# Performance work log

Hardware: AMD Instinct MI355X
Metric: run time of the kernel (lower is better)

## Reference

```python
import jax, jax.numpy as jnp
import numpy as np
from jax.scipy.special import gammaln

WARMUP = 365
KERNEL = 15
PRECISION = 1e-5

# [lo, hi] per parameter, order: BETA FC K0 K1 K2 LP PERC UZL TT CFMAX CFR CWH A THETA
PARAM_RANGES = np.array([
    [1.0, 6.0], [50.0, 1000.0], [0.05, 0.9], [0.01, 0.5], [0.001, 0.2],
    [0.2, 1.0], [0.0, 10.0], [0.0, 100.0], [-2.5, 2.5], [0.5, 10.0],
    [0.0, 0.1], [0.0, 0.2], [0.0, 2.9], [0.0, 6.5],
], dtype=np.float32)


def scale_params(parameters):
    lo = jnp.asarray(PARAM_RANGES[:, 0])
    hi = jnp.asarray(PARAM_RANGES[:, 1])
    return lo + parameters * (hi - lo)  # [n_grid, 14]


def run_hbv(p_all, pet_all, t_all, phys, init_state):
    beta, fc, k0, k1, k2 = phys[:, 0], phys[:, 1], phys[:, 2], phys[:, 3], phys[:, 4]
    lp, pperc, uzl, tt = phys[:, 5], phys[:, 6], phys[:, 7], phys[:, 8]
    cfmax, cfr, cwh = phys[:, 9], phys[:, 10], phys[:, 11]

    def step(state, inp):
        snowpack, meltwater, sm, suz, slz = state
        precip, potent, tempre = inp
        is_rain = (tempre >= tt).astype(jnp.float32)
        rain = precip * is_rain
        snow = precip * (1.0 - is_rain)
        snowpack = snowpack + snow
        melt = jnp.minimum(jnp.maximum(cfmax * (tempre - tt), 0.0), snowpack)
        meltwater = meltwater + melt
        snowpack = snowpack - melt
        refreezing = jnp.minimum(jnp.maximum(cfr * cfmax * (tt - tempre), 0.0), meltwater)
        snowpack = snowpack + refreezing
        meltwater = meltwater - refreezing
        to_soil = jnp.maximum(meltwater - cwh * snowpack, 0.0)
        meltwater = meltwater - to_soil
        soil_wetness = jnp.clip((sm / fc) ** beta, 0.0, 1.0)
        recharge = (rain + to_soil) * soil_wetness
        sm = sm + rain + to_soil - recharge
        excess = jnp.maximum(sm - fc, 0.0)
        sm = sm - excess
        evap_factor = jnp.clip(sm / (lp * fc), 0.0, 1.0)
        et_act = jnp.minimum(sm, potent * evap_factor)
        sm = jnp.maximum(sm - et_act, PRECISION)
        suz = suz + recharge + excess
        perc = jnp.minimum(suz, pperc)
        suz = suz - perc
        q0 = k0 * jnp.maximum(suz - uzl, 0.0)
        suz = suz - q0
        q1 = k1 * suz
        suz = suz - q1
        slz = slz + perc
        q2 = k2 * slz
        slz = slz - q2
        return (snowpack, meltwater, sm, suz, slz), q0 + q1 + q2

    final_state, q_sim = jax.lax.scan(step, init_state, (p_all, pet_all, t_all))
    return q_sim, final_state


def uh_gamma(a, b, len_uh):
    # a, b: [n_grid]; returns normalized gamma-pdf unit hydrograph [len_uh, n_grid]
    aa = jax.nn.relu(a) + 0.1
    theta = jax.nn.relu(b) + 0.5
    t = jnp.arange(0.5, len_uh, dtype=jnp.float32)[:, None]  # [K, 1]
    log_w = (aa - 1.0) * jnp.log(t) - t / theta - gammaln(aa) - aa * jnp.log(theta)
    w = jnp.exp(log_w)
    return w / w.sum(axis=0, keepdims=True)


def hbv_forward(x, parameters):
    n_grid = x.shape[1]
    phys = scale_params(parameters)
    init = tuple(jnp.full((n_grid,), 0.001, dtype=jnp.float32) for _ in range(5))
    # warmup under no_grad -> stop_gradient on resulting states
    xw = x[:WARMUP]
    _, warm_state = run_hbv(xw[..., 0], xw[..., 1], xw[..., 2], phys, init)
    warm_state = jax.lax.stop_gradient(warm_state)
    xm = x[WARMUP:]
    q_sim, _ = run_hbv(xm[..., 0], xm[..., 1], xm[..., 2], phys, warm_state)  # [n_step, n_grid]
    # gamma unit-hydrograph routing (causal conv over time, per grid cell)
    uh = uh_gamma(phys[:, 12], phys[:, 13], KERNEL)  # [K, n_grid]
    n_step = q_sim.shape[0]
    qp = jnp.pad(q_sim, ((KERNEL - 1, 0), (0, 0)))
    qs = jnp.zeros_like(q_sim)
    for k in range(KERNEL):
        qs = qs + uh[k] * jax.lax.dynamic_slice_in_dim(qp, KERNEL - 1 - k, n_step, 0)
    return qs[..., None]  # [n_step, n_grid, 1]


def setup_inputs() -> dict:
    key = jax.random.key(0)
    k1, k2, k3, k4 = jax.random.split(key, 4)
    T, G = 2190, 10000  # 365 warmup + 1825 simulated days, 10k basins
    precip = jax.random.uniform(k1, (T, G), dtype=jnp.float32) * 10.0  # mm/day
    pet = jax.random.uniform(k2, (T, G), dtype=jnp.float32) * 5.0      # mm/day
    temp = jax.random.normal(k3, (T, G), dtype=jnp.float32) * 10.0     # deg C
    x = jnp.stack([precip, pet, temp], axis=-1)
    parameters = jax.random.uniform(k4, (G, 14), dtype=jnp.float32)
    return {"x": x, "parameters": parameters}


def reference(x, parameters):
    return hbv_forward(x, parameters)
```

## Files before the change

### kernel.cpp

```cpp
#include <hip/hip_runtime.h>

#define WARMUP  365
#define NSTEP   1825
#define TTOT    2190
#define KERNEL_ 15
#define CH      5

__global__ __launch_bounds__(64) void hbv_fused_kernel(
    const float* __restrict__ x,
    const float* __restrict__ params,
    float* __restrict__ out,
    int G)
{
    const int g = blockIdx.x * 64 + threadIdx.x;
    if (g >= G) return;

    const float* pr = params + (size_t)g * 14;
    const float beta  = 1.0f   + pr[0]  * 5.0f;
    const float fc    = 50.0f  + pr[1]  * 950.0f;
    const float k0    = 0.05f  + pr[2]  * 0.85f;
    const float k1    = 0.01f  + pr[3]  * 0.49f;
    const float k2    = 0.001f + pr[4]  * 0.199f;
    const float lp    = 0.2f   + pr[5]  * 0.8f;
    const float pperc =          pr[6]  * 10.0f;
    const float uzl   =          pr[7]  * 100.0f;
    const float tt    = -2.5f  + pr[8]  * 5.0f;
    const float cfmax = 0.5f   + pr[9]  * 9.5f;
    const float cfr   =          pr[10] * 0.1f;
    const float cwh   =          pr[11] * 0.2f;
    const float ra    =          pr[12] * 2.9f;
    const float rb    =          pr[13] * 6.5f;

    const float aa = fmaxf(ra, 0.0f) + 0.1f;
    const float th = fmaxf(rb, 0.0f) + 0.5f;
    const float inv_th = 1.0f / th;
    float w[KERNEL_];
    float ws = 0.0f;
    #pragma unroll
    for (int k = 0; k < KERNEL_; k++) {
        const float tk = 0.5f + (float)k;
        const float lw = (aa - 1.0f) * __logf(tk) - tk * inv_th;
        w[k] = __expf(lw);
        ws += w[k];
    }
    const float inv_ws = 1.0f / ws;
    #pragma unroll
    for (int k = 0; k < KERNEL_; k++) w[k] *= inv_ws;

    const float inv_fc   = 1.0f / fc;
    const float inv_lpfc = 1.0f / (lp * fc);
    const float cfrx     = cfr * cfmax;

    float sp  = 0.001f;
    float mw  = 0.001f;
    float sm  = 0.001f;
    float suz = 0.001f;
    float slz = 0.001f;

    auto step = [&](float precip, float pet, float temp) -> float {
        const float rain = (temp >= tt) ? precip : 0.0f;
        const float snow = precip - rain;
        sp += snow;
        const float melt = fminf(fmaxf(cfmax * (temp - tt), 0.0f), sp);
        mw += melt;
        sp -= melt;
        const float refr = fminf(fmaxf(cfrx * (tt - temp), 0.0f), mw);
        sp += refr;
        mw -= refr;
        const float tosoil = fmaxf(mw - cwh * sp, 0.0f);
        mw -= tosoil;
        const float r   = sm * inv_fc;
        float wet = __expf(beta * __logf(r));
        wet = fminf(wet, 1.0f);
        const float inflow = rain + tosoil;
        const float rech   = inflow * wet;
        sm += inflow - rech;
        const float exc = fmaxf(sm - fc, 0.0f);
        sm -= exc;
        const float ef = fminf(sm * inv_lpfc, 1.0f);
        const float et = fminf(sm, pet * ef);
        sm = fmaxf(sm - et, 1e-5f);
        suz += rech + exc;
        const float perc = fminf(suz, pperc);
        suz -= perc;
        const float q0 = k0 * fmaxf(suz - uzl, 0.0f);
        suz -= q0;
        const float q1 = k1 * suz;
        suz -= q1;
        slz += perc;
        const float q2 = k2 * slz;
        slz -= q2;
        return q0 + q1 + q2;
    };

    float cur[CH][3];
    #pragma unroll
    for (int i = 0; i < CH; i++) {
        const float* p = x + ((size_t)i * G + g) * 3;
        cur[i][0] = p[0]; cur[i][1] = p[1]; cur[i][2] = p[2];
    }

    for (int tc = 0; tc < WARMUP; tc += CH) {
        float nxt[CH][3];
        #pragma unroll
        for (int i = 0; i < CH; i++) {
            const float* p = x + ((size_t)(tc + CH + i) * G + g) * 3;
            nxt[i][0] = p[0]; nxt[i][1] = p[1]; nxt[i][2] = p[2];
        }
        #pragma unroll
        for (int i = 0; i < CH; i++)
            (void)step(cur[i][0], cur[i][1], cur[i][2]);
        #pragma unroll
        for (int i = 0; i < CH; i++) {
            cur[i][0] = nxt[i][0]; cur[i][1] = nxt[i][1]; cur[i][2] = nxt[i][2];
        }
    }

    float buf[KERNEL_];
    #pragma unroll
    for (int k = 0; k < KERNEL_; k++) buf[k] = 0.0f;

    for (int tc = WARMUP; tc < TTOT; tc += CH) {
        float nxt[CH][3];
        #pragma unroll
        for (int i = 0; i < CH; i++) {
            int tn = tc + CH + i;
            if (tn > TTOT - 1) tn = TTOT - 1;
            const float* p = x + ((size_t)tn * G + g) * 3;
            nxt[i][0] = p[0]; nxt[i][1] = p[1]; nxt[i][2] = p[2];
        }
        #pragma unroll
        for (int i = 0; i < CH; i++) {
            const float q = step(cur[i][0], cur[i][1], cur[i][2]);
            #pragma unroll
            for (int k = KERNEL_ - 1; k > 0; k--) buf[k] = buf[k - 1];
            buf[0] = q;
            float acc = 0.0f;
            #pragma unroll
            for (int k = 0; k < KERNEL_; k++) acc = fmaf(w[k], buf[k], acc);
            out[(size_t)(tc - WARMUP + i) * G + g] = acc;
        }
        #pragma unroll
        for (int i = 0; i < CH; i++) {
            cur[i][0] = nxt[i][0]; cur[i][1] = nxt[i][1]; cur[i][2] = nxt[i][2];
        }
    }
}

extern "C" void kernel_launch(void* const* d_in, const int* in_sizes, int n_in,
                              void* d_out, int out_size, void* d_ws, size_t ws_size,
                              hipStream_t stream) {
    const float* x      = (const float*)d_in[0];
    const float* params = (const float*)d_in[1];
    float* out = (float*)d_out;
    const int G = in_sizes[1] / 14;
    const int blocks = (G + 63) / 64;
    hbv_fused_kernel<<<blocks, 64, 0, stream>>>(x, params, out, G);
}
```

Measured before the change: 661.9 us.

## Double-buffer 15-step input blocks and use scatter-accumulate routing ring

Replaces the 5-step prefetch with a 15-step double-buffered load scheme (A/B register blocks of 45 floats), unifying warmup and simulation into one loop of 30-step chunks. The routing convolution becomes a rotating accumulator ring updated by scattering w[k]*q forward, with constant indices under full unroll instead of a shift register and dot product. It also uses exp2/log2 builtins, folds the evapotranspiration clamp algebraically, and sets launch_bounds(64,1). The larger register footprint may cut occupancy, and the big unroll raises code size.

```diff
diff --git a/kernel.cpp b/kernel.cpp
--- a/kernel.cpp
+++ b/kernel.cpp
@@ -1,12 +1,85 @@
 #include <hip/hip_runtime.h>
 
-#define WARMUP  365
-#define NSTEP   1825
-#define TTOT    2190
-#define KERNEL_ 15
-#define CH      5
+#define WARMUP 365
+#define NSTEP  1825
+#define TTOT   2190
+#define KER    15
 
-__global__ __launch_bounds__(64) void hbv_fused_kernel(
+#define EXP2F(v) __builtin_exp2f(v)
+#define LOG2F(v) __builtin_log2f(v)
+
+#define LOADBLK(BUF, T0)                                                    \
+    do {                                                                    \
+        _Pragma("unroll")                                                   \
+        for (int j_ = 0; j_ < 15; j_++) {                                   \
+            const float* p_ = x + ((size_t)((T0) + j_) * G + g) * 3;        \
+            BUF[3 * j_ + 0] = p_[0];                                        \
+            BUF[3 * j_ + 1] = p_[1];                                        \
+            BUF[3 * j_ + 2] = p_[2];                                        \
+        }                                                                   \
+    } while (0)
+
+#define RUNBLK(BUF, TB)                                                     \
+    do {                                                                    \
+        _Pragma("unroll")                                                   \
+        for (int j = 0; j < 15; j++) {                                      \
+            const float pcp = BUF[3 * j + 0];                               \
+            const float pet = BUF[3 * j + 1];                               \
+            const float tmp = BUF[3 * j + 2];                               \
+                      \
+            const float dtemp   = tmp - tt;                                 \
+            const float rain    = (tmp >= tt) ? pcp : 0.0f;                 \
+            const float snow    = pcp - rain;                               \
+            const float meltcap = fmaxf(cfmax * dtemp, 0.0f);               \
+            const float refrcap = fmaxf(-cfrx * dtemp, 0.0f);               \
+            const float pl      = pet * inv_lpfc;                           \
+                                                       \
+            sp += snow;                                                     \
+            const float melt = fminf(meltcap, sp);                          \
+            mw += melt;                                                     \
+            sp -= melt;                                                     \
+            const float refr = fminf(refrcap, mw);                          \
+            sp += refr;                                                     \
+            mw -= refr;                                                     \
+            const float tosoil = fmaxf(mw - cwh * sp, 0.0f);                \
+            mw -= tosoil;                                                   \
+                                                         \
+            const float wet =                                               \
+                fminf(EXP2F(beta * LOG2F(sm * inv_fc)), 1.0f);              \
+            const float inflow = rain + tosoil;                             \
+            const float rech   = inflow * wet;                              \
+            const float smx    = sm + inflow;                               \
+            sm = smx - rech;                                                \
+            const float exc = fmaxf(sm - fc, 0.0f);                         \
+            sm = fminf(sm, fc);                                             \
+            const float et = fminf(sm, fminf(pl * sm, pet));                \
+            sm = fmaxf(sm - et, 1e-5f);                                     \
+                                                   \
+            suz += rech + exc;                                              \
+            const float perc = fminf(suz, pperc);                           \
+            suz -= perc;                                                    \
+            const float q0 = k0 * fmaxf(suz - uzl, 0.0f);                   \
+            suz -= q0;                                                      \
+            const float q1 = k1 * suz;                                      \
+            suz -= q1;                                                      \
+            slz += perc;                                                    \
+            const float q2 = k2 * slz;                                      \
+            slz -= q2;                                                      \
+            const float q = q0 + q1 + q2;                                   \
+                    \
+            if ((TB) + j >= WARMUP) {                                       \
+                const int s_ = (j + 10) % 15;                               \
+                out[(size_t)((TB) + j - WARMUP) * G + g] =                  \
+                    acc[s_] + w[0] * q;                                     \
+                acc[s_] = 0.0f;                                             \
+                _Pragma("unroll")                                           \
+                for (int k = 1; k < 15; k++)                                \
+                    acc[(s_ + k) % 15] += w[k] * q;                         \
+            }                                                               \
+        }                                                                   \
+    } while (0)
+
+__global__ __launch_bounds__(64, 1) void hbv_fused_kernel(
     const float* __restrict__ x,
     const float* __restrict__ params,
     float* __restrict__ out,
@@ -33,19 +106,19 @@
 
     const float aa = fmaxf(ra, 0.0f) + 0.1f;
     const float th = fmaxf(rb, 0.0f) + 0.5f;
-    const float inv_th = 1.0f / th;
-    float w[KERNEL_];
+    const float c1 = aa - 1.0f;
+    const float c2 = 1.4426950408889634f / th;
+    float w[KER];
     float ws = 0.0f;
     #pragma unroll
-    for (int k = 0; k < KERNEL_; k++) {
+    for (int k = 0; k < KER; k++) {
         const float tk = 0.5f + (float)k;
-        const float lw = (aa - 1.0f) * __logf(tk) - tk * inv_th;
-        w[k] = __expf(lw);
+        w[k] = EXP2F(c1 * LOG2F(tk) - tk * c2);
         ws += w[k];
     }
     const float inv_ws = 1.0f / ws;
     #pragma unroll
-    for (int k = 0; k < KERNEL_; k++) w[k] *= inv_ws;
+    for (int k = 0; k < KER; k++) w[k] *= inv_ws;
 
     const float inv_fc   = 1.0f / fc;
     const float inv_lpfc = 1.0f / (lp * fc);
@@ -57,93 +130,19 @@
     float suz = 0.001f;
     float slz = 0.001f;
 
-    auto step = [&](float precip, float pet, float temp) -> float {
-        const float rain = (temp >= tt) ? precip : 0.0f;
-        const float snow = precip - rain;
-        sp += snow;
-        const float melt = fminf(fmaxf(cfmax * (temp - tt), 0.0f), sp);
-        mw += melt;
-        sp -= melt;
-        const float refr = fminf(fmaxf(cfrx * (tt - temp), 0.0f), mw);
-        sp += refr;
-        mw -= refr;
-        const float tosoil = fmaxf(mw - cwh * sp, 0.0f);
-        mw -= tosoil;
-        const float r   = sm * inv_fc;
-        float wet = __expf(beta * __logf(r));
-        wet = fminf(wet, 1.0f);
-        const float inflow = rain + tosoil;
-        const float rech   = inflow * wet;
-        sm += inflow - rech;
-        const float exc = fmaxf(sm - fc, 0.0f);
-        sm -= exc;
-        const float ef = fminf(sm * inv_lpfc, 1.0f);
-        const float et = fminf(sm, pet * ef);
-        sm = fmaxf(sm - et, 1e-5f);
-        suz += rech + exc;
-        const float perc = fminf(suz, pperc);
-        suz -= perc;
-        const float q0 = k0 * fmaxf(suz - uzl, 0.0f);
-        suz -= q0;
-        const float q1 = k1 * suz;
-        suz -= q1;
-        slz += perc;
-        const float q2 = k2 * slz;
-        slz -= q2;
-        return q0 + q1 + q2;
-    };
+    float acc[KER];
+    #pragma unroll
+    for (int k = 0; k < KER; k++) acc[k] = 0.0f;
 
-    float cur[CH][3];
-    #pragma unroll
-    for (int i = 0; i < CH; i++) {
-        const float* p = x + ((size_t)i * G + g) * 3;
-        cur[i][0] = p[0]; cur[i][1] = p[1]; cur[i][2] = p[2];
-    }
-
-    for (int tc = 0; tc < WARMUP; tc += CH) {
-        float nxt[CH][3];
-        #pragma unroll
-        for (int i = 0; i < CH; i++) {
-            const float* p = x + ((size_t)(tc + CH + i) * G + g) * 3;
-            nxt[i][0] = p[0]; nxt[i][1] = p[1]; nxt[i][2] = p[2];
-        }
-        #pragma unroll
-        for (int i = 0; i < CH; i++)
-            (void)step(cur[i][0], cur[i][1], cur[i][2]);
-        #pragma unroll
-        for (int i = 0; i < CH; i++) {
-            cur[i][0] = nxt[i][0]; cur[i][1] = nxt[i][1]; cur[i][2] = nxt[i][2];
-        }
-    }
-
-    float buf[KERNEL_];
-    #pragma unroll
-    for (int k = 0; k < KERNEL_; k++) buf[k] = 0.0f;
-
-    for (int tc = WARMUP; tc < TTOT; tc += CH) {
-        float nxt[CH][3];
-        #pragma unroll
-        for (int i = 0; i < CH; i++) {
-            int tn = tc + CH + i;
-            if (tn > TTOT - 1) tn = TTOT - 1;
-            const float* p = x + ((size_t)tn * G + g) * 3;
-            nxt[i][0] = p[0]; nxt[i][1] = p[1]; nxt[i][2] = p[2];
-        }
-        #pragma unroll
-        for (int i = 0; i < CH; i++) {
-            const float q = step(cur[i][0], cur[i][1], cur[i][2]);
-            #pragma unroll
-            for (int k = KERNEL_ - 1; k > 0; k--) buf[k] = buf[k - 1];
-            buf[0] = q;
-            float acc = 0.0f;
-            #pragma unroll
-            for (int k = 0; k < KERNEL_; k++) acc = fmaf(w[k], buf[k], acc);
-            out[(size_t)(tc - WARMUP + i) * G + g] = acc;
-        }
-        #pragma unroll
-        for (int i = 0; i < CH; i++) {
-            cur[i][0] = nxt[i][0]; cur[i][1] = nxt[i][1]; cur[i][2] = nxt[i][2];
-        }
+    float A[45], B[45];
+    LOADBLK(A, 0);
+    for (int d = 0; d < 73; ++d) {
+        const int t0 = 30 * d;
+        LOADBLK(B, t0 + 15);
+        RUNBLK(A, t0);
+        const int tn = (t0 + 30 <= TTOT - 15) ? (t0 + 30) : (TTOT - 15);
+        LOADBLK(A, tn);
+        RUNBLK(B, t0 + 15);
     }
 }
 
```

New measurement: 672.2 us. No clear change (+1.6%).
